# Kernel tuning notes

Measured on AMD Instinct MI355X. Metric: run time of the kernel, lower is better.

The kernel has to match this reference:

```python
import jax, jax.numpy as jnp
import numpy as np

D, H, WIN, B, S = 768, 12, 64, 2, 1024
Dh = D // H
HALF = WIN // 2  # window covers [i-32, i+32], truncated at sequence boundaries


def setup_inputs() -> dict:
    key = jax.random.key(0)
    ks = jax.random.split(key, 16)
    def lin(k, din, dout):
        return jax.random.normal(k, (din, dout), jnp.float32) * 0.02
    inp = {"x": jax.random.normal(ks[0], (B, S, D), jnp.float32)}
    names = ["q_lin", "k_lin", "v_lin", "q_loc", "k_loc", "v_loc", "out"]
    for i, n in enumerate(names):
        inp[f"W_{n}"] = lin(ks[i + 1], D, D)
        inp[f"b_{n}"] = jnp.zeros((D,), jnp.float32)
    inp["W_g1"] = lin(ks[8], 3 * D, D); inp["b_g1"] = jnp.zeros((D,), jnp.float32)
    inp["W_g2"] = lin(ks[9], D, D);     inp["b_g2"] = jnp.zeros((D,), jnp.float32)
    inp["gamma1"] = jnp.ones((D,), jnp.float32)
    inp["beta1"] = jnp.zeros((D,), jnp.float32)
    return inp


def _layernorm(x, g, b):
    m = jnp.mean(x, axis=-1, keepdims=True)
    v = jnp.mean((x - m) ** 2, axis=-1, keepdims=True)
    return (x - m) / jnp.sqrt(v + 1e-5) * g + b


def reference(x, W_q_lin, b_q_lin, W_k_lin, b_k_lin, W_v_lin, b_v_lin,
              W_q_loc, b_q_loc, W_k_loc, b_k_loc, W_v_loc, b_v_loc,
              W_out, b_out, W_g1, b_g1, W_g2, b_g2, gamma1, beta1):
    Bc, Sc, Dc = x.shape
    residual = x
    xn = _layernorm(x, gamma1, beta1)

    # ---- linear attention branch (Katharopoulos et al. 2020) ----
    qf = jax.nn.elu(xn @ W_q_lin + b_q_lin) + 1.0
    kf = jax.nn.elu(xn @ W_k_lin + b_k_lin) + 1.0
    vl = xn @ W_v_lin + b_v_lin
    kv = jnp.einsum('bsd,bse->bde', kf, vl)            # [B,D,D]
    lin_out = jnp.einsum('bsd,bde->bse', qf, kv)       # [B,S,D]
    normalizer = jnp.einsum('bsd,bd->bs', qf, kf.sum(axis=1))
    lin_out = lin_out / (normalizer[..., None] + 1e-6)

    # ---- sliding-window attention branch (vectorized, no per-token loop) ----
    qo = (xn @ W_q_loc + b_q_loc).reshape(Bc, Sc, H, Dh)
    ko = (xn @ W_k_loc + b_k_loc).reshape(Bc, Sc, H, Dh)
    vo = (xn @ W_v_loc + b_v_loc).reshape(Bc, Sc, H, Dh)
    offsets = jnp.arange(-HALF, HALF + 1)              # [W] = 65
    idx = jnp.arange(Sc)[:, None] + offsets            # [S,W]
    valid = (idx >= 0) & (idx < Sc)                    # truncated (not clipped) window
    idxc = jnp.clip(idx, 0, Sc - 1)
    kwin = ko[:, idxc]                                 # [B,S,W,H,Dh]
    vwin = vo[:, idxc]                                 # [B,S,W,H,Dh]
    scores = jnp.einsum('bshd,bswhd->bshw', qo, kwin) / np.sqrt(Dh).astype(np.float32)
    scores = jnp.where(valid[None, :, None, :], scores, -jnp.inf)
    attn = jax.nn.softmax(scores, axis=-1)             # [B,S,H,W]
    win_out = jnp.einsum('bshw,bswhd->bshd', attn, vwin).reshape(Bc, Sc, Dc)

    # ---- adaptive gate fusion ----
    gate_in = jnp.concatenate([lin_out, win_out, xn], axis=-1)   # [B,S,3D]
    gate = jax.nn.sigmoid(jax.nn.relu(gate_in @ W_g1 + b_g1) @ W_g2 + b_g2)
    fused = gate * lin_out + (1.0 - gate) * win_out
    return fused @ W_out + b_out + residual
```

## Files before the change

### kernel.cpp

```cpp
#include <hip/hip_runtime.h>
#include <math.h>

#define DD 768
#define SS 1024
#define BB 2
#define HH 12
#define DH 64

typedef __attribute__((ext_vector_type(8))) short bf16x8;
typedef __attribute__((ext_vector_type(8))) unsigned short u16x8;
typedef __attribute__((ext_vector_type(4))) float f32x4;

constexpr size_t O_GATEIN = 0;
constexpr size_t O_WPROJT = O_GATEIN + (size_t)2048 * 2304;
constexpr size_t O_WG1T   = O_WPROJT + (size_t)4608 * 768;
constexpr size_t O_WG2T   = O_WG1T + (size_t)768 * 2304;
constexpr size_t O_WOUTT  = O_WG2T + (size_t)768 * 768;
constexpr size_t O_PROJ   = O_WOUTT + (size_t)768 * 768;
constexpr size_t O_KFT    = O_PROJ + (size_t)2048 * 4608;
constexpr size_t O_VLT    = O_KFT + (size_t)2 * 768 * 1024;
constexpr size_t O_VOT    = O_VLT + (size_t)2 * 768 * 1024;
constexpr size_t O_KVT    = O_VOT + (size_t)2 * 768 * 1024;
constexpr size_t O_H1     = O_KVT + (size_t)2 * 768 * 768;
constexpr size_t O_FUSED  = O_H1 + (size_t)2048 * 768;
constexpr size_t O_F32    = O_FUSED + (size_t)2048 * 768;

__device__ inline unsigned short f2bf(float f) {
    unsigned int u = __builtin_bit_cast(unsigned int, f);
    unsigned int r = (u + 0x7fffu + ((u >> 16) & 1u)) >> 16;
    return (unsigned short)r;
}
__device__ inline float bf2f(unsigned short h) {
    unsigned int u = ((unsigned int)h) << 16;
    return __builtin_bit_cast(float, u);
}
__device__ inline void gload16(const ushort* g, ushort* l) {
    __builtin_amdgcn_global_load_lds((const __attribute__((address_space(1))) void*)g,
                                     (__attribute__((address_space(3))) void*)l, 16, 0, 0);
}

struct PrepArgs {
    const float* src[11];
    unsigned long long dstOff[11];
    int ldo[11];
    const float* bsrc[6];
    float* bdst;
    const float* x;
    const float* gamma;
    const float* beta;
    float* kfsum;
};
__global__ __launch_bounds__(256) void prep_kernel(PrepArgs a, ushort* __restrict__ wsb) {
    __shared__ float t[64][33];
    __shared__ float ws1[4], ws2[4], mstat[2];
    int bid = blockIdx.x;
    int tid = threadIdx.x;
    if (bid < 3168) {
        int z = bid / 288;
        int rem = bid - z * 288;
        int r0 = (rem / 24) * 64, c0 = (rem % 24) * 32;
        const float* ip = a.src[z];
        ushort* op = wsb + a.dstOff[z];
        int ldo = a.ldo[z];
        #pragma unroll
        for (int k = 0; k < 8; ++k) {
            int e = k * 256 + tid;
            int row = e >> 5, col = e & 31;
            t[row][col] = ip[(size_t)(r0 + row) * 768 + c0 + col];
        }
        __syncthreads();
        #pragma unroll
        for (int k = 0; k < 8; ++k) {
            int w = k * 256 + tid;
            int cc = w >> 6, rr = w & 63;
            op[(size_t)(c0 + cc) * ldo + r0 + rr] = f2bf(t[rr][cc]);
        }
        return;
    }
    if (bid < 3186) {
        int i = (bid - 3168) * 256 + tid;
        if (i < 4608) a.bdst[i] = a.bsrc[i / 768][i % 768];
        return;
    }
    int row = bid - 3186;
    if (row == 0) {
        #pragma unroll
        for (int i = 0; i < 6; ++i) a.kfsum[tid + i * 256] = 0.f;
    }
    const float* xr = a.x + (size_t)row * DD;
    ushort* outr = wsb + O_GATEIN + (size_t)row * 2304 + 1536;
    float v[3];
    float s = 0.f, s2 = 0.f;
    #pragma unroll
    for (int r = 0; r < 3; ++r) {
        v[r] = xr[tid + r * 256];
        s += v[r];
        s2 += v[r] * v[r];
    }
    #pragma unroll
    for (int o = 32; o > 0; o >>= 1) {
        s  += __shfl_down(s, o);
        s2 += __shfl_down(s2, o);
    }
    int wid = tid >> 6, lane = tid & 63;
    if (lane == 0) { ws1[wid] = s; ws2[wid] = s2; }
    __syncthreads();
    if (tid == 0) {
        float aa = 0.f, b2 = 0.f;
        #pragma unroll
        for (int i = 0; i < 4; ++i) { aa += ws1[i]; b2 += ws2[i]; }
        float mean = aa / (float)DD;
        float var = b2 / (float)DD - mean * mean;
        mstat[0] = mean;
        mstat[1] = rsqrtf(var + 1e-5f);
    }
    __syncthreads();
    float mean = mstat[0], rstd = mstat[1];
    #pragma unroll
    for (int r = 0; r < 3; ++r) {
        int i = tid + r * 256;
        outr[i] = f2bf((v[r] - mean) * rstd * a.gamma[i] + a.beta[i]);
    }
}

template<int TM, int TN, int BK>
__device__ __forceinline__ void gemm_dev(
    ushort* lds, int bx, int by, int bz,
    const ushort* __restrict__ A, const ushort* __restrict__ B,
    ushort* __restrict__ wsb,
    float* __restrict__ Cf, ushort* __restrict__ Cb,
    const float* __restrict__ bias, const float* __restrict__ rowdiv,
    const float* __restrict__ addsrc,
    int M, int N, int K, int lda, int ldb, int ldcf, int ldcb,
    long long bA, long long bB, long long bCf, long long bCb,
    int act, int mode) {
    constexpr int MF = TM / 32;
    constexpr int NF = TN / 32;
    constexpr int TPR = BK / 8;
    constexpr int ROWS = 2048 / BK;
    constexpr int AR = TM * BK / 2048;
    constexpr int BR = TN * BK / 2048;
    constexpr int NLD = AR + BR;
    constexpr int ABUF = TM * BK;
    constexpr int BBUF = TN * BK;
    const int tid = threadIdx.x, wid = tid >> 6, lane = tid & 63;
    const int m0 = by * TM, n0 = bx * TN, z = bz;
    const ushort* Az = A + (size_t)z * bA;
    const ushort* Bz = B + (size_t)z * bB;
    const int trow = tid / TPR;
    const int ssel = (TPR >= 8) ? (trow & (TPR - 1)) : ((trow >> 1) & 3);
    const int scol = ((tid % TPR) ^ ssel) * 8;
    const int wm = wid >> 1, wn = wid & 1;
    const int fr = lane & 15, fq = lane >> 4;
    const int rsel = (TPR >= 8) ? (fr & (TPR - 1)) : ((fr >> 1) & 3);
    f32x4 acc[MF][NF];
    #pragma unroll
    for (int i = 0; i < MF; ++i)
        #pragma unroll
        for (int j = 0; j < NF; ++j) acc[i][j] = f32x4{0.f, 0.f, 0.f, 0.f};
    const int nkt = K / BK;

    auto stage = [&](int t) {
        const int k0 = t * BK;
        const int bsel = t & 1;
        #pragma unroll
        for (int i = 0; i < AR; ++i)
            gload16(Az + (size_t)(m0 + i * ROWS + trow) * lda + k0 + scol,
                    &lds[bsel * ABUF + i * 2048 + wid * 512]);
        #pragma unroll
        for (int i = 0; i < BR; ++i)
            gload16(Bz + (size_t)(n0 + i * ROWS + trow) * ldb + k0 + scol,
                    &lds[2 * ABUF + bsel * BBUF + i * 2048 + wid * 512]);
    };

    stage(0);
    for (int kt = 0; kt < nkt; ++kt) {
        if (kt + 1 < nkt) {
            stage(kt + 1);
            if constexpr (NLD == 3)      asm volatile("s_waitcnt vmcnt(3)" ::: "memory");
            else if constexpr (NLD == 4) asm volatile("s_waitcnt vmcnt(4)" ::: "memory");
            else if constexpr (NLD == 5) asm volatile("s_waitcnt vmcnt(5)" ::: "memory");
            else if constexpr (NLD == 6) asm volatile("s_waitcnt vmcnt(6)" ::: "memory");
            else                         asm volatile("s_waitcnt vmcnt(8)" ::: "memory");
        } else {
            asm volatile("s_waitcnt vmcnt(0)" ::: "memory");
        }
        __builtin_amdgcn_s_barrier();
        const ushort* As = &lds[(kt & 1) * ABUF];
        const ushort* Bs = &lds[2 * ABUF + (kt & 1) * BBUF];
        #pragma unroll
        for (int ks = 0; ks < BK / 32; ++ks) {
            const int ck = (((ks * 4 + fq) ^ rsel) << 3);
            bf16x8 af[MF], bfr[NF];
            #pragma unroll
            for (int mf = 0; mf < MF; ++mf)
                af[mf] = *(const bf16x8*)&As[(wm * (TM / 2) + mf * 16 + fr) * BK + ck];
            #pragma unroll
            for (int nf = 0; nf < NF; ++nf)
                bfr[nf] = *(const bf16x8*)&Bs[(wn * (TN / 2) + nf * 16 + fr) * BK + ck];
            #pragma unroll
            for (int mf = 0; mf < MF; ++mf)
                #pragma unroll
                for (int nf = 0; nf < NF; ++nf)
                    acc[mf][nf] = __builtin_amdgcn_mfma_f32_16x16x32_bf16(af[mf], bfr[nf], acc[mf][nf], 0, 0, 0);
        }
        asm volatile("" ::: "memory");
        __builtin_amdgcn_s_barrier();
    }

    if constexpr (TM == 64 && TN == 128) {
        if (mode == 1) {
            const int region = n0 / 768;
            const int ncol = n0 - region * 768;
            const int b = m0 >> 10, s0 = m0 & 1023;
            const bool transposed = (region == 1 || region == 2 || region == 5);
            if (!transposed) {
                #pragma unroll
                for (int mf = 0; mf < MF; ++mf) {
                    #pragma unroll
                    for (int j = 0; j < 4; ++j) {
                        int m = m0 + wm * (TM / 2) + mf * 16 + fq * 4 + j;
                        #pragma unroll
                        for (int nf = 0; nf < NF; ++nf) {
                            int n = n0 + wn * (TN / 2) + nf * 16 + fr;
                            float t = acc[mf][nf][j] + bias[n];
                            if (region == 0) t = (t > 0.f) ? t + 1.f : expf(t);
                            wsb[O_PROJ + (size_t)m * 4608 + n] = f2bf(t);
                        }
                    }
                }
            } else {
                float psum[NF];
                #pragma unroll
                for (int i = 0; i < NF; ++i) psum[i] = 0.f;
                #pragma unroll
                for (int mf = 0; mf < MF; ++mf) {
                    #pragma unroll
                    for (int nf = 0; nf < NF; ++nf) {
                        int d_l = wn * (TN / 2) + nf * 16 + fr;
                        float bs = bias[n0 + d_l];
                        #pragma unroll
                        for (int j = 0; j < 4; ++j) {
                            int s_l = wm * (TM / 2) + mf * 16 + fq * 4 + j;
                            float t = acc[mf][nf][j] + bs;
                            if (region == 1) { t = (t > 0.f) ? t + 1.f : expf(t); psum[nf] += t; }
                            lds[d_l * (TM + 8) + s_l] = f2bf(t);
                        }
                    }
                }
                if (region == 1 && rowdiv) {
                    #pragma unroll
                    for (int nf = 0; nf < NF; ++nf) {
                        float s = psum[nf];
                        s += __shfl_xor(s, 16);
                        s += __shfl_xor(s, 32);
                        if (fq == 0)
                            atomicAdd((float*)rowdiv + b * 768 + ncol + wn * (TN / 2) + nf * 16 + fr, s);
                    }
                }
                __syncthreads();
                size_t dstT = (region == 1) ? O_KFT : (region == 2) ? O_VLT : O_VOT;
                #pragma unroll
                for (int dd = 0; dd < (TN * TM / 8) / 256; ++dd) {
                    int d_l = dd * (256 / (TM / 8)) + tid / (TM / 8);
                    int sc8 = (tid % (TM / 8)) * 8;
                    u16x8 v = *(const u16x8*)&lds[d_l * (TM + 8) + sc8];
                    *(u16x8*)&wsb[dstT + (size_t)(b * 768 + ncol + d_l) * 1024 + s0 + sc8] = v;
                }
            }
            return;
        }
    }

    float* cfz = Cf ? Cf + (size_t)z * bCf : nullptr;
    ushort* cbz = Cb ? Cb + (size_t)z * bCb : nullptr;
    #pragma unroll
    for (int mf = 0; mf < MF; ++mf) {
        #pragma unroll
        for (int j = 0; j < 4; ++j) {
            int m = m0 + wm * (TM / 2) + mf * 16 + fq * 4 + j;
            float rd = rowdiv ? 1.f / (rowdiv[(size_t)z * M + m] + 1e-6f) : 1.f;
            #pragma unroll
            for (int nf = 0; nf < NF; ++nf) {
                int n = n0 + wn * (TN / 2) + nf * 16 + fr;
                float v = acc[mf][nf][j];
                if (bias) v += bias[n];
                v *= rd;
                if (act == 1) v = (v > 0.f) ? v + 1.f : expf(v);
                else if (act == 2) v = fmaxf(v, 0.f);
                else if (act == 3) v = 1.f / (1.f + expf(-v));
                if (mode == 2) {
                    float lin = bf2f(wsb[O_GATEIN + (size_t)m * 2304 + n]);
                    float win = bf2f(wsb[O_GATEIN + (size_t)m * 2304 + 768 + n]);
                    v = v * lin + (1.f - v) * win;
                }
                if (addsrc) v += addsrc[(size_t)m * ldcf + n];
                if (cfz) cfz[(size_t)m * ldcf + n] = v;
                if (cbz) cbz[(size_t)m * ldcb + n] = f2bf(v);
            }
        }
    }
}

template<int TM, int TN, int BK>
__global__ __launch_bounds__(256) void gemm_bf16(
    const ushort* __restrict__ A, const ushort* __restrict__ B,
    ushort* __restrict__ wsb,
    float* __restrict__ Cf, ushort* __restrict__ Cb,
    const float* __restrict__ bias, const float* __restrict__ rowdiv,
    const float* __restrict__ addsrc,
    int M, int N, int K, int lda, int ldb, int ldcf, int ldcb,
    long long bA, long long bB, long long bCf, long long bCb,
    int act, int mode) {
    constexpr int PIPE = 2 * TM * BK + 2 * TN * BK;
    constexpr int EPIL = (TM == 64 && TN == 128) ? 128 * (TM + 8) : 0;
    constexpr int LDSE = (PIPE > EPIL) ? PIPE : EPIL;
    __shared__ __align__(16) ushort lds[LDSE];
    int nwg = gridDim.x * gridDim.y;
    int flat = blockIdx.y * gridDim.x + blockIdx.x;
    int q = nwg >> 3;
    int nf = (flat & 7) * q + (flat >> 3);
    int bx = nf / gridDim.y;
    int by = nf % gridDim.y;
    gemm_dev<TM, TN, BK>(lds, bx, by, blockIdx.z, A, B, wsb, Cf, Cb,
                         bias, rowdiv, addsrc, M, N, K, lda, ldb, ldcf, ldcb,
                         bA, bB, bCf, bCb, act, mode);
}

__global__ __launch_bounds__(256) void kv_attn(ushort* __restrict__ wsb,
                                               const float* __restrict__ kfsum,
                                               float* __restrict__ nrm) {
    __shared__ __align__(16) ushort lds[2 * 32 * 64 + 2 * 128 * 64];
    int bid = blockIdx.x;
    int tid = threadIdx.x;
    if (bid < 288) {
        int bx = bid % 6, by = (bid / 6) % 24, bz = bid / 144;
        gemm_dev<32, 128, 64>(lds, bx, by, bz,
            wsb + O_VLT, wsb + O_KFT, wsb, nullptr, wsb + O_KVT,
            nullptr, nullptr, nullptr,
            768, 768, 1024, 1024, 1024, 0, 768,
            (long long)768 * 1024, (long long)768 * 1024, 0, (long long)768 * 768, 0, 0);
        return;
    }
    if (bid >= 672) {
        int r = tid >> 3, p = tid & 7;
        int row = (bid - 672) * 32 + r;
        int b = row >> 10;
        const ushort* qrow = wsb + O_PROJ + (size_t)row * 4608 + p * 96;
        const float* kb = kfsum + b * 768 + p * 96;
        float s = 0.f;
        #pragma unroll
        for (int i = 0; i < 96; i += 8) {
            u16x8 v = *(const u16x8*)&qrow[i];
            #pragma unroll
            for (int j = 0; j < 8; ++j) s += bf2f(v[j]) * kb[i + j];
        }
        s += __shfl_xor(s, 1);
        s += __shfl_xor(s, 2);
        s += __shfl_xor(s, 4);
        if (p == 0) nrm[row] = s;
        return;
    }
    int a = bid - 288;
    int qx = a % 16, h = (a / 16) % 12, b = a / 192;
    ushort* Ps = lds;
    int wq = tid >> 6, lane = tid & 63;
    int fq = lane >> 4, fr = lane & 15;
    int q0 = qx * 64;
    const ushort* Pb = wsb + O_PROJ + (size_t)(b * SS) * 4608;
    const ushort* Vb = wsb + O_VOT + (size_t)(b * 768 + h * 64) * 1024;
    const int qoff = 2304 + h * 64, koff = 3072 + h * 64;

    int qrow = q0 + wq * 16 + fr;
    bf16x8 aq0 = *(const bf16x8*)&Pb[(size_t)qrow * 4608 + qoff + fq * 8];
    bf16x8 aq1 = *(const bf16x8*)&Pb[(size_t)qrow * 4608 + qoff + 32 + fq * 8];

    f32x4 sc[8];
    #pragma unroll
    for (int nf = 0; nf < 8; ++nf) sc[nf] = f32x4{0.f, 0.f, 0.f, 0.f};
    #pragma unroll
    for (int nf = 0; nf < 8; ++nf) {
        int kr = q0 - 32 + nf * 16 + fr;
        int kc = kr < 0 ? 0 : (kr > 1023 ? 1023 : kr);
        bf16x8 bk0 = *(const bf16x8*)&Pb[(size_t)kc * 4608 + koff + fq * 8];
        bf16x8 bk1 = *(const bf16x8*)&Pb[(size_t)kc * 4608 + koff + 32 + fq * 8];
        sc[nf] = __builtin_amdgcn_mfma_f32_16x16x32_bf16(aq0, bk0, sc[nf], 0, 0, 0);
        sc[nf] = __builtin_amdgcn_mfma_f32_16x16x32_bf16(aq1, bk1, sc[nf], 0, 0, 0);
    }

    float p[8][4];
    float inv[4];
    #pragma unroll
    for (int j = 0; j < 4; ++j) {
        int qt = wq * 16 + fq * 4 + j;
        float sv[8];
        float mx = -1e30f;
        #pragma unroll
        for (int nf = 0; nf < 8; ++nf) {
            int c = nf * 16 + fr;
            int kg = q0 - 32 + c;
            bool val = (c >= qt) && (c <= qt + 64) && (kg >= 0) && (kg < SS);
            float t = sc[nf][j] * 0.125f;
            sv[nf] = val ? t : -1e30f;
            mx = fmaxf(mx, sv[nf]);
        }
        mx = fmaxf(mx, __shfl_xor(mx, 1));
        mx = fmaxf(mx, __shfl_xor(mx, 2));
        mx = fmaxf(mx, __shfl_xor(mx, 4));
        mx = fmaxf(mx, __shfl_xor(mx, 8));
        float dn = 0.f;
        #pragma unroll
        for (int nf = 0; nf < 8; ++nf) {
            float e = expf(sv[nf] - mx);
            p[nf][j] = e;
            dn += e;
        }
        dn += __shfl_xor(dn, 1);
        dn += __shfl_xor(dn, 2);
        dn += __shfl_xor(dn, 4);
        dn += __shfl_xor(dn, 8);
        inv[j] = 1.f / dn;
    }

    #pragma unroll
    for (int nf = 0; nf < 8; ++nf) {
        int chunk = nf * 2 + (fr >> 3);
        #pragma unroll
        for (int j = 0; j < 4; ++j) {
            int r = fq * 4 + j;
            Ps[wq * 2048 + r * 128 + ((chunk ^ r) * 8) + (fr & 7)] = f2bf(p[nf][j] * inv[j]);
        }
    }
    __syncthreads();

    f32x4 oa[4];
    #pragma unroll
    for (int nf = 0; nf < 4; ++nf) oa[nf] = f32x4{0.f, 0.f, 0.f, 0.f};
    #pragma unroll
    for (int ks = 0; ks < 4; ++ks) {
        bf16x8 pa = *(const bf16x8*)&Ps[wq * 2048 + fr * 128 + (((ks * 4 + fq) ^ fr) * 8)];
        #pragma unroll
        for (int nf = 0; nf < 4; ++nf) {
            int dr = nf * 16 + fr;
            const ushort* vp = Vb + (ptrdiff_t)dr * 1024 + (q0 - 32 + ks * 32 + fq * 8);
            bf16x8 bv = *(const bf16x8*)vp;
            oa[nf] = __builtin_amdgcn_mfma_f32_16x16x32_bf16(pa, bv, oa[nf], 0, 0, 0);
        }
    }

    #pragma unroll
    for (int nf = 0; nf < 4; ++nf) {
        int d = nf * 16 + fr;
        #pragma unroll
        for (int j = 0; j < 4; ++j) {
            int q = q0 + wq * 16 + fq * 4 + j;
            wsb[O_GATEIN + (size_t)(b * SS + q) * 2304 + 768 + h * 64 + d] = f2bf(oa[nf][j]);
        }
    }
}

extern "C" void kernel_launch(void* const* d_in, const int* in_sizes, int n_in,
                              void* d_out, int out_size, void* d_ws, size_t ws_size,
                              hipStream_t stream) {
    const float* x      = (const float*)d_in[0];
    const float* W_q    = (const float*)d_in[1];
    const float* b_q    = (const float*)d_in[2];
    const float* W_k    = (const float*)d_in[3];
    const float* b_k    = (const float*)d_in[4];
    const float* W_v    = (const float*)d_in[5];
    const float* b_v    = (const float*)d_in[6];
    const float* W_ql   = (const float*)d_in[7];
    const float* b_ql   = (const float*)d_in[8];
    const float* W_kl   = (const float*)d_in[9];
    const float* b_kl   = (const float*)d_in[10];
    const float* W_vl   = (const float*)d_in[11];
    const float* b_vl   = (const float*)d_in[12];
    const float* W_out  = (const float*)d_in[13];
    const float* b_out  = (const float*)d_in[14];
    const float* W_g1   = (const float*)d_in[15];
    const float* b_g1   = (const float*)d_in[16];
    const float* W_g2   = (const float*)d_in[17];
    const float* b_g2   = (const float*)d_in[18];
    const float* gamma1 = (const float*)d_in[19];
    const float* beta1  = (const float*)d_in[20];

    ushort* wsb = (ushort*)d_ws;
    float* f32a = (float*)(wsb + O_F32);
    float* bias_cat = f32a;
    float* kfsum    = f32a + 4608;
    float* nrm      = kfsum + 1536;

    const long long W2 = (long long)768 * 768;

    PrepArgs pa;
    const float* wsrc[6] = {W_q, W_k, W_v, W_ql, W_kl, W_vl};
    for (int i = 0; i < 6; ++i) { pa.src[i] = wsrc[i]; pa.dstOff[i] = O_WPROJT + i * W2; pa.ldo[i] = 768; }
    for (int i = 0; i < 3; ++i) { pa.src[6 + i] = W_g1 + (size_t)i * 768 * 768; pa.dstOff[6 + i] = O_WG1T + i * 768; pa.ldo[6 + i] = 2304; }
    pa.src[9] = W_g2;  pa.dstOff[9] = O_WG2T;  pa.ldo[9] = 768;
    pa.src[10] = W_out; pa.dstOff[10] = O_WOUTT; pa.ldo[10] = 768;
    const float* bsrc[6] = {b_q, b_k, b_v, b_ql, b_kl, b_vl};
    for (int i = 0; i < 6; ++i) pa.bsrc[i] = bsrc[i];
    pa.bdst = bias_cat;
    pa.x = x; pa.gamma = gamma1; pa.beta = beta1;
    pa.kfsum = kfsum;
    prep_kernel<<<dim3(5234), 256, 0, stream>>>(pa, wsb);

    gemm_bf16<64, 128, 64><<<dim3(36, 32, 1), 256, 0, stream>>>(
        wsb + O_GATEIN + 1536, wsb + O_WPROJT, wsb, nullptr, nullptr, bias_cat, kfsum, nullptr,
        2048, 4608, 768, 2304, 768, 0, 0, 0, 0, 0, 0, 0, 1);

    kv_attn<<<dim3(736), 256, 0, stream>>>(wsb, kfsum, nrm);

    gemm_bf16<32, 64, 64><<<dim3(12, 32, 2), 256, 0, stream>>>(
        wsb + O_PROJ, wsb + O_KVT, wsb, nullptr, wsb + O_GATEIN, nullptr, nrm, nullptr,
        1024, 768, 768, 4608, 768, 0, 2304,
        (long long)1024 * 4608, W2, 0, (long long)1024 * 2304, 0, 0);

    gemm_bf16<32, 64, 64><<<dim3(12, 64, 1), 256, 0, stream>>>(
        wsb + O_GATEIN, wsb + O_WG1T, wsb, nullptr, wsb + O_H1, b_g1, nullptr, nullptr,
        2048, 768, 2304, 2304, 2304, 0, 768, 0, 0, 0, 0, 2, 0);

    gemm_bf16<32, 64, 64><<<dim3(12, 64, 1), 256, 0, stream>>>(
        wsb + O_H1, wsb + O_WG2T, wsb, nullptr, wsb + O_FUSED, b_g2, nullptr, nullptr,
        2048, 768, 768, 768, 768, 0, 768, 0, 0, 0, 0, 3, 2);

    gemm_bf16<32, 64, 64><<<dim3(12, 64, 1), 256, 0, stream>>>(
        wsb + O_FUSED, wsb + O_WOUTT, wsb, (float*)d_out, nullptr, b_out, nullptr, x,
        2048, 768, 768, 768, 768, 768, 0, 0, 0, (long long)0, 0, 0, 0);
}
```

Before: 109.9 us.

## Merge back-half kernels into one cooperative persistent kernel with grid syncs

```diff
diff --git a/kernel.cpp b/kernel.cpp
--- a/kernel.cpp
+++ b/kernel.cpp
@@ -1,4 +1,5 @@
 #include <hip/hip_runtime.h>
+#include <hip/hip_cooperative_groups.h>
 #include <math.h>
 
 #define DD 768
@@ -6,6 +7,8 @@
 #define BB 2
 #define HH 12
 #define DH 64
+
+namespace cg = cooperative_groups;
 
 typedef __attribute__((ext_vector_type(8))) short bf16x8;
 typedef __attribute__((ext_vector_type(8))) unsigned short u16x8;
@@ -327,11 +330,10 @@
                          bA, bB, bCf, bCb, act, mode);
 }
 
-__global__ __launch_bounds__(256) void kv_attn(ushort* __restrict__ wsb,
-                                               const float* __restrict__ kfsum,
-                                               float* __restrict__ nrm) {
-    __shared__ __align__(16) ushort lds[2 * 32 * 64 + 2 * 128 * 64];
-    int bid = blockIdx.x;
+__device__ __forceinline__ void kv_attn_body(ushort* lds, int bid,
+                                             ushort* __restrict__ wsb,
+                                             const float* __restrict__ kfsum,
+                                             float* __restrict__ nrm) {
     int tid = threadIdx.x;
     if (bid < 288) {
         int bx = bid % 6, by = (bid / 6) % 24, bz = bid / 144;
@@ -457,6 +459,51 @@
             wsb[O_GATEIN + (size_t)(b * SS + q) * 2304 + 768 + h * 64 + d] = f2bf(oa[nf][j]);
         }
     }
+}
+
+__global__ __launch_bounds__(256) void kv_attn(ushort* __restrict__ wsb,
+                                               const float* __restrict__ kfsum,
+                                               float* __restrict__ nrm) {
+    __shared__ __align__(16) ushort lds[2 * 32 * 64 + 2 * 128 * 64];
+    kv_attn_body(lds, blockIdx.x, wsb, kfsum, nrm);
+}
+
+__global__ __launch_bounds__(256, 3) void back_kernel(
+    ushort* __restrict__ wsb, const float* __restrict__ kfsum, float* __restrict__ nrm,
+    const float* __restrict__ b_g1, const float* __restrict__ b_g2,
+    const float* __restrict__ b_out, const float* __restrict__ x,
+    float* __restrict__ out) {
+    __shared__ __align__(16) ushort lds[2 * 32 * 64 + 2 * 128 * 64];
+    cg::grid_group grid = cg::this_grid();
+    const int bid = blockIdx.x;
+    const long long W2 = (long long)768 * 768;
+
+    if (bid < 736) kv_attn_body(lds, bid, wsb, kfsum, nrm);
+    grid.sync();
+
+    gemm_dev<32, 64, 64>(lds, bid % 12, (bid / 12) % 32, bid / 384,
+        wsb + O_PROJ, wsb + O_KVT, wsb, nullptr, wsb + O_GATEIN,
+        nullptr, nrm, nullptr,
+        1024, 768, 768, 4608, 768, 0, 2304,
+        (long long)1024 * 4608, W2, 0, (long long)1024 * 2304, 0, 0);
+    grid.sync();
+
+    gemm_dev<32, 64, 64>(lds, bid % 12, bid / 12, 0,
+        wsb + O_GATEIN, wsb + O_WG1T, wsb, nullptr, wsb + O_H1,
+        b_g1, nullptr, nullptr,
+        2048, 768, 2304, 2304, 2304, 0, 768, 0, 0, 0, 0, 2, 0);
+    grid.sync();
+
+    gemm_dev<32, 64, 64>(lds, bid % 12, bid / 12, 0,
+        wsb + O_H1, wsb + O_WG2T, wsb, nullptr, wsb + O_FUSED,
+        b_g2, nullptr, nullptr,
+        2048, 768, 768, 768, 768, 0, 768, 0, 0, 0, 0, 3, 2);
+    grid.sync();
+
+    gemm_dev<32, 64, 64>(lds, bid % 12, bid / 12, 0,
+        wsb + O_FUSED, wsb + O_WOUTT, wsb, out, nullptr,
+        b_out, nullptr, x,
+        2048, 768, 768, 768, 768, 768, 0, 0, 0, 0, 0, 0, 0);
 }
 
 extern "C" void kernel_launch(void* const* d_in, const int* in_sizes, int n_in,
@@ -509,22 +556,31 @@
         wsb + O_GATEIN + 1536, wsb + O_WPROJT, wsb, nullptr, nullptr, bias_cat, kfsum, nullptr,
         2048, 4608, 768, 2304, 768, 0, 0, 0, 0, 0, 0, 0, 1);
 
-    kv_attn<<<dim3(736), 256, 0, stream>>>(wsb, kfsum, nrm);
-
-    gemm_bf16<32, 64, 64><<<dim3(12, 32, 2), 256, 0, stream>>>(
-        wsb + O_PROJ, wsb + O_KVT, wsb, nullptr, wsb + O_GATEIN, nullptr, nrm, nullptr,
-        1024, 768, 768, 4608, 768, 0, 2304,
-        (long long)1024 * 4608, W2, 0, (long long)1024 * 2304, 0, 0);
-
-    gemm_bf16<32, 64, 64><<<dim3(12, 64, 1), 256, 0, stream>>>(
-        wsb + O_GATEIN, wsb + O_WG1T, wsb, nullptr, wsb + O_H1, b_g1, nullptr, nullptr,
-        2048, 768, 2304, 2304, 2304, 0, 768, 0, 0, 0, 0, 2, 0);
-
-    gemm_bf16<32, 64, 64><<<dim3(12, 64, 1), 256, 0, stream>>>(
-        wsb + O_H1, wsb + O_WG2T, wsb, nullptr, wsb + O_FUSED, b_g2, nullptr, nullptr,
-        2048, 768, 768, 768, 768, 0, 768, 0, 0, 0, 0, 3, 2);
-
-    gemm_bf16<32, 64, 64><<<dim3(12, 64, 1), 256, 0, stream>>>(
-        wsb + O_FUSED, wsb + O_WOUTT, wsb, (float*)d_out, nullptr, b_out, nullptr, x,
-        2048, 768, 768, 768, 768, 768, 0, 0, 0, (long long)0, 0, 0, 0);
-}
+    float* outp = (float*)d_out;
+    int nb = 0;
+    hipError_t qerr = hipOccupancyMaxActiveBlocksPerMultiprocessor(
+        &nb, reinterpret_cast<const void*>(back_kernel), 256, 0);
+    bool coop = (qerr == hipSuccess && nb >= 3);
+    hipError_t lerr = hipErrorUnknown;
+    if (coop) {
+        void* kargs[] = {&wsb, &kfsum, &nrm, &b_g1, &b_g2, &b_out, &x, &outp};
+        lerr = hipLaunchCooperativeKernel(reinterpret_cast<void*>(back_kernel),
+                                          dim3(768), dim3(256), kargs, 0, stream);
+    }
+    if (!coop || lerr != hipSuccess) {
+        kv_attn<<<dim3(736), 256, 0, stream>>>(wsb, kfsum, nrm);
+        gemm_bf16<32, 64, 64><<<dim3(12, 32, 2), 256, 0, stream>>>(
+            wsb + O_PROJ, wsb + O_KVT, wsb, nullptr, wsb + O_GATEIN, nullptr, nrm, nullptr,
+            1024, 768, 768, 4608, 768, 0, 2304,
+            (long long)1024 * 4608, W2, 0, (long long)1024 * 2304, 0, 0);
+        gemm_bf16<32, 64, 64><<<dim3(12, 64, 1), 256, 0, stream>>>(
+            wsb + O_GATEIN, wsb + O_WG1T, wsb, nullptr, wsb + O_H1, b_g1, nullptr, nullptr,
+            2048, 768, 2304, 2304, 2304, 0, 768, 0, 0, 0, 0, 2, 0);
+        gemm_bf16<32, 64, 64><<<dim3(12, 64, 1), 256, 0, stream>>>(
+            wsb + O_H1, wsb + O_WG2T, wsb, nullptr, wsb + O_FUSED, b_g2, nullptr, nullptr,
+            2048, 768, 768, 768, 768, 0, 768, 0, 0, 0, 0, 3, 2);
+        gemm_bf16<32, 64, 64><<<dim3(12, 64, 1), 256, 0, stream>>>(
+            wsb + O_FUSED, wsb + O_WOUTT, wsb, (float*)d_out, nullptr, b_out, nullptr, x,
+            2048, 768, 768, 768, 768, 768, 0, 0, 0, (long long)0, 0, 0, 0);
+    }
+}
```

Result: no change. 110.2 us (+0.3%).
